# Kernel optimization log

Measured on AMD Instinct MI355X. Metric: run time of the kernel, lower is better.

## Reference

```python
import jax, jax.numpy as jnp
import numpy as np

DIM = 1024
STATE = 256
B, S = 4, 4096

def setup_inputs() -> dict:
    key = jax.random.key(0)
    ks = jax.random.split(key, 8)
    sc_b = 1.0 / np.sqrt(DIM)
    sc_c = 1.0 / np.sqrt(STATE)
    return {
        "x": jax.random.normal(ks[0], (B, S, DIM), dtype=jnp.float32),
        "A": jax.random.normal(ks[1], (STATE,), dtype=jnp.float32) * 0.02,
        "B_w": jax.random.uniform(ks[2], (STATE, DIM), minval=-sc_b, maxval=sc_b),
        "B_b": jax.random.uniform(ks[3], (STATE,), minval=-sc_b, maxval=sc_b),
        "C_w": jax.random.uniform(ks[4], (DIM, STATE), minval=-sc_c, maxval=sc_c),
        "C_b": jax.random.uniform(ks[5], (DIM,), minval=-sc_c, maxval=sc_c),
        "D_w": jax.random.uniform(ks[6], (DIM, DIM), minval=-sc_b, maxval=sc_b),
        "D_b": jax.random.uniform(ks[7], (DIM,), minval=-sc_b, maxval=sc_b),
    }

def reference(x, A, B_w, B_b, C_w, C_b, D_w, D_b):
    # Precompute input projections in batch (the per-step loop only needs state*A + Bu)
    Bu = jnp.einsum('bsd,nd->bsn', x, B_w) + B_b          # [B,S,STATE]
    Du = jnp.einsum('bsd,ed->bse', x, D_w) + D_b          # [B,S,DIM]
    Aexp = jnp.exp(A)[None, :]                             # [1,STATE]
    state0 = jnp.zeros((x.shape[0], A.shape[0]), dtype=x.dtype)

    def step(state, bu_t):
        state = jnp.tanh(state * Aexp + bu_t)
        return state, state

    _, states = jax.lax.scan(step, state0, jnp.swapaxes(Bu, 0, 1))  # [S,B,STATE]
    states = jnp.swapaxes(states, 0, 1)                              # [B,S,STATE]
    y = jnp.einsum('bsn,en->bse', states, C_w) + C_b + Du
    return y
```

## Files before the change

### kernel.cpp

```cpp
#include <hip/hip_runtime.h>
#include <hip/hip_bf16.h>

#define DIM 1024
#define STATE 256
#define BATCH 4
#define SEQ 4096
#define M_TOT (BATCH * SEQ)

typedef short short8 __attribute__((ext_vector_type(8)));
typedef float f32x4 __attribute__((ext_vector_type(4)));

__device__ __forceinline__ unsigned short f2bf(float f) {
  unsigned int u = __float_as_uint(f);
  u += 0x7fff + ((u >> 16) & 1);
  return (unsigned short)(u >> 16);
}

__device__ __forceinline__ float bf2f(unsigned short u) {
  return __uint_as_float((unsigned int)u << 16);
}

__device__ __forceinline__ void gl_lds16(const void* g, void* l) {
  __builtin_amdgcn_global_load_lds(
      (const __attribute__((address_space(1))) void*)g,
      (__attribute__((address_space(3))) void*)l, 16, 0, 0);
}

#define C2F 2.8853900817779268f
#define LOG2EF 1.4426950408889634f
#define VMC(N) asm volatile("s_waitcnt vmcnt(" #N ")" ::: "memory")

__global__ __launch_bounds__(256) void convert_bw(
    const float* __restrict__ Bw, unsigned short* __restrict__ bwb) {
  const int r = blockIdx.x;
  const int c = threadIdx.x * 4;
  const float4 v = *(const float4*)(Bw + (size_t)r * DIM + c);
  *(ushort4*)(bwb + (size_t)r * DIM + c) =
      make_ushort4(f2bf(v.x), f2bf(v.y), f2bf(v.z), f2bf(v.w));
}

__global__ __launch_bounds__(256, 2) void gemm_GX(
    const float* __restrict__ x,
    const unsigned short* __restrict__ bwb,
    const float* __restrict__ Bb,
    const float* __restrict__ A,
    unsigned short* __restrict__ G,
    unsigned short* __restrict__ xb)
{
  __shared__ char lds[81920];

  const int tid = threadIdx.x;
  const int wave = tid >> 6;
  const int lane = tid & 63;
  const int lr = lane & 15;
  const int lk = lane >> 4;
  const int m0 = blockIdx.x * 32;

  f32x4 acc[2][4];
#pragma unroll
  for (int i = 0; i < 2; ++i)
#pragma unroll
    for (int j = 0; j < 4; ++j) acc[i][j] = (f32x4){0.f, 0.f, 0.f, 0.f};

  const char* xB  = (const char*)x;
  const char* bwB = (const char*)bwb;
  char* xbB = (char*)xb;

  auto stage = [&](int kt) {
    if (kt >= 16) return;
    char* slot = lds + (kt & 1) * 40960;
#pragma unroll
    for (int i = 0; i < 2; ++i) {
      const int s = i * 256 + tid;
      const int r = s >> 4;
      const int c = (s & 15) ^ (r & 7);
      gl_lds16(xB + (size_t)(m0 + r) * 4096 + (size_t)kt * 256 + c * 16,
               slot + i * 4096 + wave * 1024);
    }
#pragma unroll
    for (int i = 0; i < 8; ++i) {
      const int s = i * 256 + tid;
      const int r = s >> 3;
      const int c = (s & 7) ^ (r & 7);
      gl_lds16(bwB + (size_t)r * 2048 + (size_t)kt * 128 + c * 16,
               slot + 8192 + i * 4096 + wave * 1024);
    }
  };

  stage(0);
  VMC(0);
  __builtin_amdgcn_s_barrier();
  stage(1);

  for (int t = 0; t < 16; ++t) {
    const char* As = lds + (t & 1) * 40960;
    const char* Bs = As + 8192;

    short8 af[2][2];
#pragma unroll
    for (int kk = 0; kk < 2; ++kk)
#pragma unroll
      for (int f = 0; f < 2; ++f) {
        const int row = f * 16 + lr;
        const int sw = row & 7;
        const f32x4 a0 = *(const f32x4*)(As + row * 256 + (((kk * 8 + 2 * lk)     ^ sw) << 4));
        const f32x4 a1 = *(const f32x4*)(As + row * 256 + (((kk * 8 + 2 * lk + 1) ^ sw) << 4));
        short8 v;
#pragma unroll
        for (int j = 0; j < 4; ++j) {
          v[j]     = (short)f2bf(a0[j]);
          v[4 + j] = (short)f2bf(a1[j]);
        }
        af[kk][f] = v;
      }
    short8 bfr[2][4];
#pragma unroll
    for (int kk = 0; kk < 2; ++kk)
#pragma unroll
      for (int fj = 0; fj < 4; ++fj) {
        const int n = wave * 64 + fj * 16 + lr;
        bfr[kk][fj] = *(const short8*)(Bs + n * 128 + (((kk * 4 + lk) ^ (n & 7)) << 4));
      }
#pragma unroll
    for (int kk = 0; kk < 2; ++kk)
#pragma unroll
      for (int f = 0; f < 2; ++f)
#pragma unroll
        for (int fj = 0; fj < 4; ++fj)
          acc[f][fj] = __builtin_amdgcn_mfma_f32_16x16x32_bf16(
              af[kk][f], bfr[kk][fj], acc[f][fj], 0, 0, 0);

    if ((t & 3) == wave) {
#pragma unroll
      for (int kk = 0; kk < 2; ++kk)
#pragma unroll
        for (int f = 0; f < 2; ++f) {
          const int row = f * 16 + lr;
          *(short8*)(xbB + (size_t)(m0 + row) * 2048 +
                     (size_t)t * 128 + kk * 64 + lk * 16) = af[kk][f];
        }
    }

    if (t < 15) {
      VMC(0);
      __builtin_amdgcn_s_barrier();
      stage(t + 2);
    }
  }

#pragma unroll
  for (int fj = 0; fj < 4; ++fj) {
    const int cg = wave * 64 + fj * 16 + lr;
    const float bbv = fmaf(Bb[cg], C2F,
                           C2F * __builtin_amdgcn_exp2f(A[cg] * LOG2EF));
#pragma unroll
    for (int f = 0; f < 2; ++f)
#pragma unroll
      for (int j = 0; j < 4; ++j) {
        const int rg = m0 + f * 16 + lk * 4 + j;
        G[(size_t)rg * STATE + cg] = f2bf(fmaf(acc[f][fj][j], C2F, bbv));
      }
  }
}

__global__ __launch_bounds__(256) void scan_kernel(
    const unsigned short* __restrict__ G,
    const float* __restrict__ A,
    const float* __restrict__ Cw,
    const float* __restrict__ Dw,
    unsigned short* __restrict__ wob,
    unsigned short* __restrict__ states)
{
  const int tid = threadIdx.x;
  const int e0 = blockIdx.x * 4;
#pragma unroll
  for (int rr = 0; rr < 4; ++rr) {
    const int e = e0 + rr;
    if (tid < 64) {
      const float4 v = *(const float4*)(Cw + (size_t)e * STATE + tid * 4);
      *(ushort4*)(wob + (size_t)e * 1280 + tid * 4) =
          make_ushort4(f2bf(v.x), f2bf(v.y), f2bf(v.z), f2bf(v.w));
    }
    const float4 v = *(const float4*)(Dw + (size_t)e * DIM + tid * 4);
    *(ushort4*)(wob + (size_t)e * 1280 + 256 + tid * 4) =
        make_ushort4(f2bf(v.x), f2bf(v.y), f2bf(v.z), f2bf(v.w));
  }

  const int b = blockIdx.x >> 6;
  const int chunk = blockIdx.x & 63;
  const int n = tid;
  const int t0 = chunk * 64;
  const int start = (t0 > 64) ? (t0 - 64) : 0;
  const int nw = t0 - start;
  const int total = nw + 64;

  const unsigned short* g = G + ((size_t)b * SEQ + start) * STATE + n;
  unsigned short* q = states + ((size_t)b * SEQ + start) * STATE + n;
  const float P = C2F * __builtin_amdgcn_exp2f(A[n] * LOG2EF);
  const float mP2 = -2.0f * P;

  float r = 0.5f;
  constexpr int CH = 16;
  float cur[CH], nxt[CH];
#pragma unroll
  for (int j = 0; j < CH; ++j) cur[j] = bf2f(g[(size_t)j * STATE]);

  const int NC = total / CH;
  for (int c = 0; c < NC; ++c) {
    if (c + 1 < NC) {
      const unsigned short* pn = g + (size_t)(c + 1) * CH * STATE;
#pragma unroll
      for (int j = 0; j < CH; ++j) nxt[j] = bf2f(pn[(size_t)j * STATE]);
    }
    if (c * CH >= nw) {
      unsigned short* qc = q + (size_t)c * CH * STATE;
#pragma unroll
      for (int j = 0; j < CH; ++j) {
        const float t = fmaf(mP2, r, cur[j]);
        const float e = __builtin_amdgcn_exp2f(t);
        r = __builtin_amdgcn_rcpf(1.0f + e);
        const float s = fmaf(-2.0f, r, 1.0f);
        qc[(size_t)j * STATE] = f2bf(s);
      }
    } else {
#pragma unroll
      for (int j = 0; j < CH; ++j) {
        const float t = fmaf(mP2, r, cur[j]);
        const float e = __builtin_amdgcn_exp2f(t);
        r = __builtin_amdgcn_rcpf(1.0f + e);
      }
    }
    if (c + 1 < NC) {
#pragma unroll
      for (int j = 0; j < CH; ++j) cur[j] = nxt[j];
    }
  }
}

#define PH(TILE, Q, STG, VMST)                                                 \
  do {                                                                         \
    const char* As = lds + ((TILE) & 1) * 32768;                               \
    const char* Bs = lds + 65536 + ((TILE) & 1) * 32768;                       \
    if ((Q) == 0) {                                                            \
      _Pragma("unroll") for (int fj = 0; fj < 4; ++fj) {                       \
        const int r = wn * 64 + fj * 16 + lr;                                  \
        _Pragma("unroll") for (int kk = 0; kk < 2; ++kk)                       \
          bfr[fj][kk] = *(const short8*)(Bs + r * 128 +                        \
                                         (((kk * 4 + lk) ^ (r & 7)) << 4));    \
      }                                                                        \
    }                                                                          \
    short8 af[2][2];                                                           \
    _Pragma("unroll") for (int fl = 0; fl < 2; ++fl) {                         \
      const int r = wm * 128 + (Q) * 32 + fl * 16 + lr;                        \
      _Pragma("unroll") for (int kk = 0; kk < 2; ++kk)                         \
        af[fl][kk] = *(const short8*)(As + r * 128 +                           \
                                      (((kk * 4 + lk) ^ (r & 7)) << 4));       \
    }                                                                          \
    STG;                                                                       \
    if ((Q) == 0) asm volatile("s_waitcnt lgkmcnt(8)" ::: "memory");           \
    __builtin_amdgcn_s_barrier();                                              \
    __builtin_amdgcn_s_setprio(1);                                             \
    _Pragma("unroll") for (int kk = 0; kk < 2; ++kk)                           \
      _Pragma("unroll") for (int fl = 0; fl < 2; ++fl)                         \
        _Pragma("unroll") for (int fj = 0; fj < 4; ++fj)                       \
          acc[(Q) * 2 + fl][fj] = __builtin_amdgcn_mfma_f32_16x16x32_bf16(     \
              af[fl][kk], bfr[fj][kk], acc[(Q) * 2 + fl][fj], 0, 0, 0);        \
    __builtin_amdgcn_s_setprio(0);                                             \
    VMST;                                                                      \
    __builtin_amdgcn_s_barrier();                                              \
  } while (0)

__global__ __launch_bounds__(512, 2) void gemm_out(
    const unsigned short* __restrict__ stb,
    const unsigned short* __restrict__ xb,
    const unsigned short* __restrict__ wob,
    const float* __restrict__ Cb,
    const float* __restrict__ Db,
    float* __restrict__ dout)
{
  __shared__ char lds[131072];

  const int tid = threadIdx.x;
  const int wave = tid >> 6;
  const int lane = tid & 63;
  const int lr = lane & 15;
  const int lk = lane >> 4;
  const int wm = wave >> 2;
  const int wn = wave & 3;

  const int bs = ((blockIdx.x & 7) << 5) | (blockIdx.x >> 3);
  const int m0 = (bs >> 2) * 256;
  const int n0 = (bs & 3) * 256;

  const char* stbB = (const char*)stb;
  const char* xbB  = (const char*)xb;
  const char* wobB = (const char*)wob;

  f32x4 acc[8][4];
#pragma unroll
  for (int i = 0; i < 8; ++i)
#pragma unroll
    for (int j = 0; j < 4; ++j) acc[i][j] = (f32x4){0.f, 0.f, 0.f, 0.f};

  auto stageA = [&](int kt, int h) {
    if (kt >= 20) return;
    const char* base;
    size_t str;
    size_t colb;
    if (kt < 4) { base = stbB; str = 512;  colb = (size_t)kt * 128; }
    else        { base = xbB;  str = 2048; colb = (size_t)(kt - 4) * 128; }
    base += (size_t)m0 * str;
#pragma unroll
    for (int i2 = 0; i2 < 2; ++i2) {
      const int s = i2 * 512 + tid;
      const int r = s >> 3;
      const int cl = (s & 7) ^ (r & 7);
      gl_lds16(base + (size_t)(h * 128 + r) * str + colb + cl * 16,
               lds + ((kt & 1) * 32768) + h * 16384 + i2 * 8192 + wave * 1024);
    }
  };
  auto stageB = [&](int kt, int h) {
    if (kt >= 20) return;
#pragma unroll
    for (int i2 = 0; i2 < 2; ++i2) {
      const int s = i2 * 512 + tid;
      const int r = s >> 3;
      const int cl = (s & 7) ^ (r & 7);
      gl_lds16(wobB + (size_t)(n0 + h * 128 + r) * 2560 + (size_t)kt * 128 + cl * 16,
               lds + 65536 + ((kt & 1) * 32768) + h * 16384 + i2 * 8192 + wave * 1024);
    }
  };

  stageA(0, 0); stageA(0, 1);
  stageB(0, 0); stageB(0, 1);
  stageB(1, 0); stageB(1, 1);
  VMC(4);
  __builtin_amdgcn_s_barrier();

  short8 bfr[4][2];
  for (int i = 0; i < 10; ++i) {
    const int e = 2 * i, o = e + 1;
    PH(e, 0, stageA(o, 0), );
    PH(e, 1, stageA(o, 1), );
    PH(e, 2, stageB(e + 2, 0), );
    PH(e, 3, stageB(e + 2, 1), if (i == 9) { VMC(0); } else { VMC(4); });
    PH(o, 0, stageA(e + 2, 0), );
    PH(o, 1, stageA(e + 2, 1), );
    PH(o, 2, stageB(o + 2, 0), );
    PH(o, 3, stageB(o + 2, 1), VMC(4));
  }

#pragma unroll
  for (int fj = 0; fj < 4; ++fj) {
    const int col = n0 + wn * 64 + fj * 16 + lr;
    const float cb = Cb[col] + Db[col];
#pragma unroll
    for (int m = 0; m < 8; ++m) {
      const int rowb = m0 + wm * 128 + m * 16 + lk * 4;
#pragma unroll
      for (int j = 0; j < 4; ++j)
        dout[(size_t)(rowb + j) * DIM + col] = acc[m][fj][j] + cb;
    }
  }
}

extern "C" void kernel_launch(void* const* d_in, const int* in_sizes, int n_in,
                              void* d_out, int out_size, void* d_ws, size_t ws_size,
                              hipStream_t stream) {
  const float* x  = (const float*)d_in[0];
  const float* A  = (const float*)d_in[1];
  const float* Bw = (const float*)d_in[2];
  const float* Bb = (const float*)d_in[3];
  const float* Cw = (const float*)d_in[4];
  const float* Cb = (const float*)d_in[5];
  const float* Dw = (const float*)d_in[6];
  const float* Db = (const float*)d_in[7];
  float* dout = (float*)d_out;

  char* ws = (char*)d_ws;
  unsigned short* xb   = (unsigned short*)(ws);
  unsigned short* bwb  = (unsigned short*)(ws + 33554432);
  unsigned short* wob  = (unsigned short*)(ws + 34078720);
  unsigned short* G    = (unsigned short*)(ws + 36700160);
  unsigned short* stb  = (unsigned short*)(ws + 53477376);

  convert_bw<<<256, 256, 0, stream>>>(Bw, bwb);
  gemm_GX<<<512, 256, 0, stream>>>(x, bwb, Bb, A, G, xb);
  scan_kernel<<<BATCH * 64, 256, 0, stream>>>(G, A, Cw, Dw, wob, stb);
  gemm_out<<<256, 512, 0, stream>>>(stb, xb, wob, Cb, Db, dout);
}
```

Measured before the change: 91.82 us.

## Shrink gemm_out tile to 128x256 with single-buffered LDS and more blocks

Replaces the 256x256 double-buffered, finely interleaved 8-phase pipeline in the output GEMM with a 128x256 tile, single-buffered 48KB LDS, and a simple load-barrier-compute loop. The grid doubles to 512 blocks and launch bounds request 4 blocks per CU, aiming for more occupancy and better CU coverage. In exchange it loses the overlap of global-to-LDS loads with MFMA work (each step waits with vmcnt(0)) and reuses the B tile less.

```diff
diff --git a/kernel.cpp b/kernel.cpp
--- a/kernel.cpp
+++ b/kernel.cpp
@@ -237,40 +237,7 @@
   }
 }
 
-#define PH(TILE, Q, STG, VMST)                                                 \
-  do {                                                                         \
-    const char* As = lds + ((TILE) & 1) * 32768;                               \
-    const char* Bs = lds + 65536 + ((TILE) & 1) * 32768;                       \
-    if ((Q) == 0) {                                                            \
-      _Pragma("unroll") for (int fj = 0; fj < 4; ++fj) {                       \
-        const int r = wn * 64 + fj * 16 + lr;                                  \
-        _Pragma("unroll") for (int kk = 0; kk < 2; ++kk)                       \
-          bfr[fj][kk] = *(const short8*)(Bs + r * 128 +                        \
-                                         (((kk * 4 + lk) ^ (r & 7)) << 4));    \
-      }                                                                        \
-    }                                                                          \
-    short8 af[2][2];                                                           \
-    _Pragma("unroll") for (int fl = 0; fl < 2; ++fl) {                         \
-      const int r = wm * 128 + (Q) * 32 + fl * 16 + lr;                        \
-      _Pragma("unroll") for (int kk = 0; kk < 2; ++kk)                         \
-        af[fl][kk] = *(const short8*)(As + r * 128 +                           \
-                                      (((kk * 4 + lk) ^ (r & 7)) << 4));       \
-    }                                                                          \
-    STG;                                                                       \
-    if ((Q) == 0) asm volatile("s_waitcnt lgkmcnt(8)" ::: "memory");           \
-    __builtin_amdgcn_s_barrier();                                              \
-    __builtin_amdgcn_s_setprio(1);                                             \
-    _Pragma("unroll") for (int kk = 0; kk < 2; ++kk)                           \
-      _Pragma("unroll") for (int fl = 0; fl < 2; ++fl)                         \
-        _Pragma("unroll") for (int fj = 0; fj < 4; ++fj)                       \
-          acc[(Q) * 2 + fl][fj] = __builtin_amdgcn_mfma_f32_16x16x32_bf16(     \
-              af[fl][kk], bfr[fj][kk], acc[(Q) * 2 + fl][fj], 0, 0, 0);        \
-    __builtin_amdgcn_s_setprio(0);                                             \
-    VMST;                                                                      \
-    __builtin_amdgcn_s_barrier();                                              \
-  } while (0)
-
-__global__ __launch_bounds__(512, 2) void gemm_out(
+__global__ __launch_bounds__(512, 4) void gemm_out(
     const unsigned short* __restrict__ stb,
     const unsigned short* __restrict__ xb,
     const unsigned short* __restrict__ wob,
@@ -278,7 +245,7 @@
     const float* __restrict__ Db,
     float* __restrict__ dout)
 {
-  __shared__ char lds[131072];
+  __shared__ char lds[49152];
 
   const int tid = threadIdx.x;
   const int wave = tid >> 6;
@@ -288,66 +255,80 @@
   const int wm = wave >> 2;
   const int wn = wave & 3;
 
-  const int bs = ((blockIdx.x & 7) << 5) | (blockIdx.x >> 3);
-  const int m0 = (bs >> 2) * 256;
+  const int bs = ((blockIdx.x & 7) << 6) | (blockIdx.x >> 3);
+  const int m0 = (bs >> 2) * 128;
   const int n0 = (bs & 3) * 256;
 
   const char* stbB = (const char*)stb;
   const char* xbB  = (const char*)xb;
   const char* wobB = (const char*)wob;
 
-  f32x4 acc[8][4];
-#pragma unroll
-  for (int i = 0; i < 8; ++i)
+  f32x4 acc[4][4];
+#pragma unroll
+  for (int i = 0; i < 4; ++i)
 #pragma unroll
     for (int j = 0; j < 4; ++j) acc[i][j] = (f32x4){0.f, 0.f, 0.f, 0.f};
 
-  auto stageA = [&](int kt, int h) {
+  auto stage = [&](int kt) {
     if (kt >= 20) return;
-    const char* base;
-    size_t str;
-    size_t colb;
-    if (kt < 4) { base = stbB; str = 512;  colb = (size_t)kt * 128; }
-    else        { base = xbB;  str = 2048; colb = (size_t)(kt - 4) * 128; }
-    base += (size_t)m0 * str;
+    const char* abase;
+    size_t astr, acolb;
+    if (kt < 4) { abase = stbB; astr = 512;  acolb = (size_t)kt * 128; }
+    else        { abase = xbB;  astr = 2048; acolb = (size_t)(kt - 4) * 128; }
+    abase += (size_t)m0 * astr;
 #pragma unroll
     for (int i2 = 0; i2 < 2; ++i2) {
       const int s = i2 * 512 + tid;
       const int r = s >> 3;
       const int cl = (s & 7) ^ (r & 7);
-      gl_lds16(base + (size_t)(h * 128 + r) * str + colb + cl * 16,
-               lds + ((kt & 1) * 32768) + h * 16384 + i2 * 8192 + wave * 1024);
-    }
-  };
-  auto stageB = [&](int kt, int h) {
-    if (kt >= 20) return;
-#pragma unroll
-    for (int i2 = 0; i2 < 2; ++i2) {
+      gl_lds16(abase + (size_t)r * astr + acolb + cl * 16,
+               lds + i2 * 8192 + wave * 1024);
+    }
+#pragma unroll
+    for (int i2 = 0; i2 < 4; ++i2) {
       const int s = i2 * 512 + tid;
       const int r = s >> 3;
       const int cl = (s & 7) ^ (r & 7);
-      gl_lds16(wobB + (size_t)(n0 + h * 128 + r) * 2560 + (size_t)kt * 128 + cl * 16,
-               lds + 65536 + ((kt & 1) * 32768) + h * 16384 + i2 * 8192 + wave * 1024);
+      gl_lds16(wobB + (size_t)(n0 + r) * 2560 + (size_t)kt * 128 + cl * 16,
+               lds + 16384 + i2 * 8192 + wave * 1024);
     }
   };
 
-  stageA(0, 0); stageA(0, 1);
-  stageB(0, 0); stageB(0, 1);
-  stageB(1, 0); stageB(1, 1);
-  VMC(4);
+  stage(0);
+  VMC(0);
   __builtin_amdgcn_s_barrier();
 
-  short8 bfr[4][2];
-  for (int i = 0; i < 10; ++i) {
-    const int e = 2 * i, o = e + 1;
-    PH(e, 0, stageA(o, 0), );
-    PH(e, 1, stageA(o, 1), );
-    PH(e, 2, stageB(e + 2, 0), );
-    PH(e, 3, stageB(e + 2, 1), if (i == 9) { VMC(0); } else { VMC(4); });
-    PH(o, 0, stageA(e + 2, 0), );
-    PH(o, 1, stageA(e + 2, 1), );
-    PH(o, 2, stageB(o + 2, 0), );
-    PH(o, 3, stageB(o + 2, 1), VMC(4));
+  const char* As = lds;
+  const char* Bs = lds + 16384;
+  for (int t = 0; t < 20; ++t) {
+#pragma unroll
+    for (int kk = 0; kk < 2; ++kk) {
+      short8 af[4], bfr[4];
+#pragma unroll
+      for (int fi = 0; fi < 4; ++fi) {
+        const int r = wm * 64 + fi * 16 + lr;
+        af[fi] = *(const short8*)(As + r * 128 + (((kk * 4 + lk) ^ (r & 7)) << 4));
+      }
+#pragma unroll
+      for (int fj = 0; fj < 4; ++fj) {
+        const int r = wn * 64 + fj * 16 + lr;
+        bfr[fj] = *(const short8*)(Bs + r * 128 + (((kk * 4 + lk) ^ (r & 7)) << 4));
+      }
+      __builtin_amdgcn_s_setprio(1);
+#pragma unroll
+      for (int fi = 0; fi < 4; ++fi)
+#pragma unroll
+        for (int fj = 0; fj < 4; ++fj)
+          acc[fi][fj] = __builtin_amdgcn_mfma_f32_16x16x32_bf16(
+              af[fi], bfr[fj], acc[fi][fj], 0, 0, 0);
+      __builtin_amdgcn_s_setprio(0);
+    }
+    __builtin_amdgcn_s_barrier();
+    if (t < 19) {
+      stage(t + 1);
+      VMC(0);
+      __builtin_amdgcn_s_barrier();
+    }
   }
 
 #pragma unroll
@@ -355,11 +336,11 @@
     const int col = n0 + wn * 64 + fj * 16 + lr;
     const float cb = Cb[col] + Db[col];
 #pragma unroll
-    for (int m = 0; m < 8; ++m) {
-      const int rowb = m0 + wm * 128 + m * 16 + lk * 4;
+    for (int fi = 0; fi < 4; ++fi) {
+      const int rowb = m0 + wm * 64 + fi * 16 + lk * 4;
 #pragma unroll
       for (int j = 0; j < 4; ++j)
-        dout[(size_t)(rowb + j) * DIM + col] = acc[m][fj][j] + cb;
+        dout[(size_t)(rowb + j) * DIM + col] = acc[fi][fj][j] + cb;
     }
   }
 }
@@ -387,5 +368,5 @@
   convert_bw<<<256, 256, 0, stream>>>(Bw, bwb);
   gemm_GX<<<512, 256, 0, stream>>>(x, bwb, Bb, A, G, xb);
   scan_kernel<<<BATCH * 64, 256, 0, stream>>>(G, A, Cw, Dw, wob, stb);
-  gemm_out<<<256, 512, 0, stream>>>(stb, xb, wob, Cb, Db, dout);
-}
+  gemm_out<<<512, 512, 0, stream>>>(stb, xb, wob, Cb, Db, dout);
+}
```

Result: slower. 100.8 us (+9.8%).
